# Kernel optimization log

Hardware: AMD Instinct MI355X
Metric: run time of the kernel (lower is better)

## Reference

```python
import jax, jax.numpy as jnp
import numpy as np

N = 100_000      # nodes
E = 1_600_000    # edges (avg degree 16)
D = 128          # emb_dim
L = 2            # num_layer
BN_EPS = 1e-5


def setup_inputs() -> dict:
    key = jax.random.key(0)
    ks = jax.random.split(key, 16)
    s = 0.05
    inp = {
        # int inputs
        "x": jax.random.randint(ks[0], (N, 9), 0, 2),
        "z": jax.random.randint(ks[1], (N,), 0, 1000),
        "edge_index": jax.random.randint(ks[2], (2, E), 0, N),
        "edge_attr": jax.random.randint(ks[3], (E, 3), 0, 2),
        # learned params
        "atom_emb": jax.random.normal(ks[4], (9, 119, D), jnp.float32) * s,  # padded stacked AtomEncoder tables
        "z_emb": jax.random.normal(ks[5], (1000, D), jnp.float32) * s,
        "bond_emb": jax.random.normal(ks[6], (L, 3, 6, D), jnp.float32) * s,  # padded BondEncoder tables per layer
        "eps": jnp.zeros((L,), jnp.float32),
        "W1": jax.random.normal(ks[7], (L, D, 2 * D), jnp.float32) * s,
        "b1": jnp.zeros((L, 2 * D), jnp.float32),
        "g1": jnp.ones((L, 2 * D), jnp.float32),
        "be1": jnp.zeros((L, 2 * D), jnp.float32),
        "W2": jax.random.normal(ks[8], (L, 2 * D, D), jnp.float32) * s,
        "b2": jnp.zeros((L, D), jnp.float32),
        "bng": jnp.ones((L, D), jnp.float32),
        "bnb": jnp.zeros((L, D), jnp.float32),
    }
    return inp


def _batchnorm(h, g, b):
    # training-mode BatchNorm1d: batch stats, biased variance
    m = h.mean(axis=0)
    v = h.var(axis=0)
    return (h - m) * jax.lax.rsqrt(v + BN_EPS) * g + b


def _multi_embed(tables, idx):
    # tables: [F, V, D], idx: [N, F] -> sum_f tables[f][idx[:, f]]  -> [N, D]
    return jax.vmap(lambda t, i: t[i], in_axes=(0, 1))(tables, idx).sum(axis=0)


def reference(x, z, edge_index, edge_attr, atom_emb, z_emb, bond_emb, eps,
              W1, b1, g1, be1, W2, b2, bng, bnb):
    src, dst = edge_index[0], edge_index[1]
    # h0 = AtomEncoder(x) + z_embedding(z)
    h = _multi_embed(atom_emb, x) + z_emb[z]
    for l in range(L):
        # GINConv: bond encode -> gather -> relu message -> scatter-add -> MLP
        e_emb = _multi_embed(bond_emb[l], edge_attr)          # [E, D]
        msg = jax.nn.relu(h[src] + e_emb)                      # [E, D]
        agg = jax.ops.segment_sum(msg, dst, num_segments=N)    # [N, D]
        pre = (1.0 + eps[l]) * h + agg
        hid = jax.nn.relu(_batchnorm(pre @ W1[l] + b1[l], g1[l], be1[l]))
        hconv = hid @ W2[l] + b2[l]
        h = _batchnorm(hconv, bng[l], bnb[l])
        if l < L - 1:
            h = jax.nn.relu(h)   # dropout ratio 0 -> identity
    return h
```

## Files before the change

### kernel.cpp

```cpp
#include <hip/hip_runtime.h>

#define D 128
#define BN_EPS 1e-5f
#define NSUB 1024
#define CAP2 2048

typedef __attribute__((ext_vector_type(8))) short short8;
typedef __attribute__((ext_vector_type(4))) float floatx4;

__device__ __forceinline__ float bf2f(unsigned short u) {
    unsigned int x = ((unsigned int)u) << 16;
    return __builtin_bit_cast(float, x);
}
__device__ __forceinline__ unsigned short f2bf(float f) {
    unsigned int x = __builtin_bit_cast(unsigned int, f);
    x = x + 0x7FFFu + ((x >> 16) & 1u);
    return (unsigned short)(x >> 16);
}

__global__ void node_init_kernel(const int* __restrict__ x, const int* __restrict__ z,
                                 const float* __restrict__ atom_emb,
                                 const float* __restrict__ z_emb,
                                 unsigned short* __restrict__ hb, int N) {
    int gid = blockIdx.x * blockDim.x + threadIdx.x;
    int node = gid >> 5;
    if (node >= N) return;
    int d0 = (gid & 31) * 4;
    float4 acc = *(const float4*)(z_emb + (size_t)z[node] * D + d0);
#pragma unroll
    for (int f = 0; f < 9; ++f) {
        int v = x[node * 9 + f];
        const float4 t = *(const float4*)(atom_emb + (size_t)(f * 119 + v) * D + d0);
        acc.x += t.x; acc.y += t.y; acc.z += t.z; acc.w += t.w;
    }
    ushort4 o;
    o.x = f2bf(acc.x); o.y = f2bf(acc.y); o.z = f2bf(acc.z); o.w = f2bf(acc.w);
    *(ushort4*)(hb + (size_t)node * D + d0) = o;
}

__global__ __launch_bounds__(256)
void partition1_kernel(const int* __restrict__ ei, const int* __restrict__ ea,
                       int2* __restrict__ l1, int* __restrict__ tail1,
                       int E, int N, int capE, int ntiles, int nblocks) {
    __shared__ int lcnt[8], lbase[8];
    const int tid = threadIdx.x;
    for (int tile = blockIdx.x; tile < ntiles; tile += nblocks) {
        const int tb = tile * 4096;
        if (tid < 8) lcnt[tid] = 0;
        __syncthreads();
        int mydst[16], mypay[16];
#pragma unroll
        for (int j = 0; j < 16; ++j) {
            int e = tb + j * 256 + tid;
            if (e < E) {
                int dst = ei[E + e];
                int c = (ea[3 * e] * 6 + ea[3 * e + 1]) * 6 + ea[3 * e + 2];
                mydst[j] = dst;
                mypay[j] = ei[e] | (c << 17);
                atomicAdd(&lcnt[(int)((8LL * dst) / N)], 1);
            } else {
                mydst[j] = -1;
            }
        }
        __syncthreads();
        if (tid < 8) {
            lbase[tid] = atomicAdd(&tail1[tid], lcnt[tid]);
            lcnt[tid] = 0;
        }
        __syncthreads();
#pragma unroll
        for (int j = 0; j < 16; ++j) {
            if (mydst[j] >= 0) {
                int s = (int)((8LL * mydst[j]) / N);
                int pos = lbase[s] + atomicAdd(&lcnt[s], 1);
                if (pos < capE) l1[(size_t)s * capE + pos] = make_int2(mydst[j], mypay[j]);
            }
        }
        __syncthreads();
    }
}

__global__ __launch_bounds__(256)
void partition2_kernel(const int2* __restrict__ l1, const int* __restrict__ tail1,
                       unsigned int* __restrict__ subL, int* __restrict__ tail2,
                       int N, int capE, int G) {
    __shared__ int lcnt[128], lbase[128];
    const int s = blockIdx.x & 7;
    const int g = blockIdx.x >> 3;
    const int tid = threadIdx.x;
    const int len = min(tail1[s], capE);
    const int2* src = l1 + (size_t)s * capE;
    for (int tb = g * 4096; tb < len; tb += G * 4096) {
        if (tid < 128) lcnt[tid] = 0;
        __syncthreads();
        int2 e[16];
        int sub[16];
#pragma unroll
        for (int j = 0; j < 16; ++j) {
            int i = tb + j * 256 + tid;
            if (i < len) {
                e[j] = src[i];
                sub[j] = (int)((1024LL * e[j].x) / N) - (s << 7);
                atomicAdd(&lcnt[sub[j]], 1);
            } else {
                sub[j] = -1;
            }
        }
        __syncthreads();
        if (tid < 128) {
            lbase[tid] = atomicAdd(&tail2[(s << 7) + tid], lcnt[tid]);
            lcnt[tid] = 0;
        }
        __syncthreads();
#pragma unroll
        for (int j = 0; j < 16; ++j) {
            if (sub[j] >= 0) {
                int k = (s << 7) + sub[j];
                int lo = (int)(((long long)k * N + 1023) >> 10);
                int pos = lbase[sub[j]] + atomicAdd(&lcnt[sub[j]], 1);
                if (pos < CAP2)
                    subL[(size_t)k * CAP2 + pos] =
                        (unsigned int)e[j].y | ((unsigned int)(e[j].x - lo) << 25);
            }
        }
        __syncthreads();
    }
}

__global__ __launch_bounds__(1024)
void subscan_kernel(const int* __restrict__ tail2, int* __restrict__ subbase,
                    int* __restrict__ offsets, int N) {
    const int tid = threadIdx.x, lane = tid & 63, wid = tid >> 6;
    int v = min(tail2[tid], CAP2);
    int s = v;
#pragma unroll
    for (int off = 1; off < 64; off <<= 1) {
        int t = __shfl_up(s, off, 64);
        if (lane >= off) s += t;
    }
    __shared__ int ws[16];
    if (lane == 63) ws[wid] = s;
    __syncthreads();
    if (wid == 0) {
        int w = (lane < 16) ? ws[lane] : 0;
#pragma unroll
        for (int off = 1; off < 16; off <<= 1) {
            int t = __shfl_up(w, off, 64);
            if (lane >= off) w += t;
        }
        if (lane < 16) ws[lane] = w;
    }
    __syncthreads();
    int excl = (wid ? ws[wid - 1] : 0) + s - v;
    subbase[tid] = excl;
    if (tid == 1023) offsets[N] = excl + v;
}

__global__ __launch_bounds__(256)
void csr_sort_kernel(const unsigned int* __restrict__ subL, const int* __restrict__ tail2,
                     const int* __restrict__ subbase, int* __restrict__ offsets,
                     int* __restrict__ bucket, int N) {
    const int k = blockIdx.x;
    const int tid = threadIdx.x, lane = tid & 63, wid = tid >> 6;
    const int len = min(tail2[k], CAP2);
    const int base = subbase[k];
    const int lo = (int)(((long long)k * N + 1023) >> 10);
    const int hi = (int)(((long long)(k + 1) * N + 1023) >> 10);
    const int nn = hi - lo;
    __shared__ int cnt[128], loff[128], wsum[4];
    __shared__ unsigned int sorted[CAP2];
    const unsigned int* src = subL + (size_t)k * CAP2;

    if (tid < 128) cnt[tid] = 0;
    __syncthreads();
    for (int i = tid; i < len; i += 256) atomicAdd(&cnt[src[i] >> 25], 1);
    __syncthreads();
    int v = (tid < 128) ? cnt[tid] : 0;
    int s = v;
#pragma unroll
    for (int off = 1; off < 64; off <<= 1) {
        int t = __shfl_up(s, off, 64);
        if (lane >= off) s += t;
    }
    if (lane == 63) wsum[wid] = s;
    __syncthreads();
    if (tid < 128) loff[tid] = ((wid == 1) ? wsum[0] : 0) + s - v;
    __syncthreads();
    if (tid < nn) offsets[lo + tid] = base + loff[tid];
    if (tid < 128) cnt[tid] = 0;
    __syncthreads();
    for (int i = tid; i < len; i += 256) {
        unsigned int e = src[i];
        int ld = e >> 25;
        int pos = loff[ld] + atomicAdd(&cnt[ld], 1);
        sorted[pos] = e & 0x1FFFFFFu;
    }
    __syncthreads();
    for (int i = tid; i < len; i += 256) bucket[base + i] = (int)sorted[i];
}

__global__ void comb_kernel(const float* __restrict__ bond_emb, unsigned short* __restrict__ comb) {
    int idx = blockIdx.x * 256 + threadIdx.x;
    if (idx >= 216 * D) return;
    int c = idx >> 7, d = idx & 127;
    int a0 = c / 36, a1 = (c / 6) % 6, a2 = c % 6;
    const float* b = bond_emb + (size_t)blockIdx.y * 3 * 6 * D;
    float v = b[(0 * 6 + a0) * D + d] + b[(1 * 6 + a1) * D + d] + b[(2 * 6 + a2) * D + d];
    comb[(size_t)blockIdx.y * 216 * D + idx] = f2bf(v);
}

__global__ void pack_w_kernel(const float* __restrict__ W, unsigned short* __restrict__ Wp,
                              int total, int logN) {
    int idx = blockIdx.x * 256 + threadIdx.x;
    if (idx >= total) return;
    int NCOLS = 1 << logN;
    int k = idx >> logN, n = idx & (NCOLS - 1);
    int k0 = k >> 5, kq = k & 31, q = kq >> 3, j = kq & 7;
    int t = n >> 4, ln = n & 15;
    size_t dest = (((size_t)k0 * (NCOLS >> 4) + t) << 9) + ((q << 4) + ln) * 8 + j;
    const float* Wl = W + (size_t)blockIdx.y * total;
    unsigned short* Wpl = Wp + (size_t)blockIdx.y * total;
    Wpl[dest] = f2bf(Wl[idx]);
}

__global__ __launch_bounds__(256)
void gather_reduce_kernel(const int* __restrict__ offsets, const int* __restrict__ bucket,
                          const unsigned short* __restrict__ comb,
                          const unsigned short* __restrict__ hb,
                          const float* __restrict__ eps_l,
                          unsigned short* __restrict__ pre, int N) {
    int gid = blockIdx.x * blockDim.x + threadIdx.x;
    int node = gid >> 4;
    if (node >= N) return;
    int d0 = (gid & 15) * 8;

    union U8 { int4 i; unsigned short u[8]; };
    float s = 1.0f + eps_l[0];
    float a[8];
    {
        U8 hv; hv.i = *(const int4*)(hb + (size_t)node * D + d0);
#pragma unroll
        for (int j = 0; j < 8; ++j) a[j] = bf2f(hv.u[j]) * s;
    }
    const int beg = offsets[node], end = offsets[node + 1];
    for (int p = beg; p < end; p += 4) {
        int rem = end - p;
        int pk0 = bucket[p];
        int pk1 = bucket[rem > 1 ? p + 1 : p];
        int pk2 = bucket[rem > 2 ? p + 2 : p];
        int pk3 = bucket[rem > 3 ? p + 3 : p];
        U8 h0, h1, h2, h3, c0, c1, c2, c3;
        h0.i = *(const int4*)(hb + (size_t)(pk0 & 0x1FFFF) * D + d0);
        c0.i = *(const int4*)(comb + (size_t)((pk0 >> 17) & 0xFF) * D + d0);
        h1.i = *(const int4*)(hb + (size_t)(pk1 & 0x1FFFF) * D + d0);
        c1.i = *(const int4*)(comb + (size_t)((pk1 >> 17) & 0xFF) * D + d0);
        h2.i = *(const int4*)(hb + (size_t)(pk2 & 0x1FFFF) * D + d0);
        c2.i = *(const int4*)(comb + (size_t)((pk2 >> 17) & 0xFF) * D + d0);
        h3.i = *(const int4*)(hb + (size_t)(pk3 & 0x1FFFF) * D + d0);
        c3.i = *(const int4*)(comb + (size_t)((pk3 >> 17) & 0xFF) * D + d0);
#pragma unroll
        for (int j = 0; j < 8; ++j) a[j] += fmaxf(bf2f(h0.u[j]) + bf2f(c0.u[j]), 0.0f);
        if (rem > 1) {
#pragma unroll
            for (int j = 0; j < 8; ++j) a[j] += fmaxf(bf2f(h1.u[j]) + bf2f(c1.u[j]), 0.0f);
        }
        if (rem > 2) {
#pragma unroll
            for (int j = 0; j < 8; ++j) a[j] += fmaxf(bf2f(h2.u[j]) + bf2f(c2.u[j]), 0.0f);
        }
        if (rem > 3) {
#pragma unroll
            for (int j = 0; j < 8; ++j) a[j] += fmaxf(bf2f(h3.u[j]) + bf2f(c3.u[j]), 0.0f);
        }
    }
    U8 o;
#pragma unroll
    for (int j = 0; j < 8; ++j) o.u[j] = f2bf(a[j]);
    *(int4*)(pre + (size_t)node * D + d0) = o.i;
}

template <int K, int NCOLS, int TRANSFORM, int OUTBF>
__global__ __launch_bounds__(256)
void mfma_gemm_kernel(const unsigned short* __restrict__ A,
                      const unsigned short* __restrict__ Wp,
                      const float* __restrict__ bias,
                      const float* __restrict__ tscale, const float* __restrict__ tshift,
                      unsigned short* __restrict__ Cbf, float* __restrict__ Cf,
                      float* __restrict__ partial, int M) {
    constexpr int NT = NCOLS / 16;
    constexpr int NCHUNK = K / 32;
    constexpr int CPP = NCHUNK / 2;
    __shared__ unsigned short Ws[16384];
    __shared__ float red[NCOLS * 2];

    const int tid = threadIdx.x;
    const int wave = tid >> 6, lane = tid & 63;
    const int quad = lane >> 4, ln = lane & 15;
    const int m_base = blockIdx.x * 64 + wave * 16;
    int arow = m_base + ln;
    if (arow >= M) arow = M - 1;
    const int kq = quad * 8;

    int4 araw[NCHUNK];
#pragma unroll
    for (int c = 0; c < NCHUNK; ++c)
        araw[c] = *(const int4*)(A + (size_t)arow * K + c * 32 + kq);

    for (int i = tid; i < NCOLS * 2; i += 256) red[i] = 0.f;

    floatx4 acc[NT];
#pragma unroll
    for (int t = 0; t < NT; ++t) acc[t] = (floatx4){0.f, 0.f, 0.f, 0.f};

#pragma unroll
    for (int ph = 0; ph < 2; ++ph) {
        if (ph) __syncthreads();
#pragma unroll
        for (int i = 0; i < 16384; i += 2048)
            *(int4*)&Ws[i + tid * 8] = *(const int4*)&Wp[ph * 16384 + i + tid * 8];
        __syncthreads();
#pragma unroll
        for (int cc = 0; cc < CPP; ++cc) {
            const int c = ph * CPP + cc;
            short8 afrag;
            if constexpr (TRANSFORM) {
                union { int4 i; unsigned short u[8]; } raw;
                raw.i = araw[c];
                const int kb = c * 32 + kq;
                float4 sc0 = *(const float4*)(tscale + kb);
                float4 sc1 = *(const float4*)(tscale + kb + 4);
                float4 sh0 = *(const float4*)(tshift + kb);
                float4 sh1 = *(const float4*)(tshift + kb + 4);
                union { short8 v; unsigned short u[8]; } au;
                au.u[0] = f2bf(fmaxf(bf2f(raw.u[0]) * sc0.x + sh0.x, 0.f));
                au.u[1] = f2bf(fmaxf(bf2f(raw.u[1]) * sc0.y + sh0.y, 0.f));
                au.u[2] = f2bf(fmaxf(bf2f(raw.u[2]) * sc0.z + sh0.z, 0.f));
                au.u[3] = f2bf(fmaxf(bf2f(raw.u[3]) * sc0.w + sh0.w, 0.f));
                au.u[4] = f2bf(fmaxf(bf2f(raw.u[4]) * sc1.x + sh1.x, 0.f));
                au.u[5] = f2bf(fmaxf(bf2f(raw.u[5]) * sc1.y + sh1.y, 0.f));
                au.u[6] = f2bf(fmaxf(bf2f(raw.u[6]) * sc1.z + sh1.z, 0.f));
                au.u[7] = f2bf(fmaxf(bf2f(raw.u[7]) * sc1.w + sh1.w, 0.f));
                afrag = au.v;
            } else {
                afrag = __builtin_bit_cast(short8, araw[c]);
            }
#pragma unroll
            for (int t = 0; t < NT; ++t) {
                short8 bfrag = *(const short8*)&Ws[(((cc * NT) + t) << 9) + lane * 8];
                acc[t] = __builtin_amdgcn_mfma_f32_16x16x32_bf16(afrag, bfrag, acc[t], 0, 0, 0);
            }
        }
    }

#pragma unroll
    for (int t = 0; t < NT; ++t) {
        int col = t * 16 + ln;
        float bv = bias[col];
        float sv = 0.f, qv = 0.f;
#pragma unroll
        for (int r = 0; r < 4; ++r) {
            int row = m_base + quad * 4 + r;
            if (row < M) {
                float v = acc[t][r] + bv;
                sv += v; qv += v * v;
                if constexpr (OUTBF) Cbf[(size_t)row * NCOLS + col] = f2bf(v);
                else                 Cf[(size_t)row * NCOLS + col] = v;
            }
        }
        sv += __shfl_xor(sv, 16, 64); sv += __shfl_xor(sv, 32, 64);
        qv += __shfl_xor(qv, 16, 64); qv += __shfl_xor(qv, 32, 64);
        if (quad == 0) {
            atomicAdd(&red[col], sv);
            atomicAdd(&red[NCOLS + col], qv);
        }
    }
    __syncthreads();
    float* pout = partial + (size_t)blockIdx.x * (NCOLS * 2);
    for (int i = tid; i < NCOLS * 2; i += 256) pout[i] = red[i];
}

template <int NCOLS>
__global__ __launch_bounds__(256)
void reduce_stats_kernel(const float* __restrict__ partial, int nb,
                         const float* __restrict__ g, const float* __restrict__ b,
                         float* __restrict__ scale, float* __restrict__ shift, float invN) {
    const int col = blockIdx.x;
    const int tid = threadIdx.x;
    float s = 0.f, q = 0.f;
    for (int bb = tid; bb < nb; bb += 256) {
        const float* p = partial + (size_t)bb * (NCOLS * 2);
        s += p[col];
        q += p[NCOLS + col];
    }
#pragma unroll
    for (int off = 32; off > 0; off >>= 1) {
        s += __shfl_xor(s, off, 64);
        q += __shfl_xor(q, off, 64);
    }
    __shared__ float ws[4], wq[4];
    if ((tid & 63) == 0) { ws[tid >> 6] = s; wq[tid >> 6] = q; }
    __syncthreads();
    if (tid == 0) {
        s = ws[0] + ws[1] + ws[2] + ws[3];
        q = wq[0] + wq[1] + wq[2] + wq[3];
        float mean = s * invN;
        float var = q * invN - mean * mean;
        float inv = 1.0f / sqrtf(var + BN_EPS);
        float sc = g[col] * inv;
        scale[col] = sc;
        shift[col] = b[col] - mean * sc;
    }
}

__global__ void bn_apply_kernel(const float* __restrict__ X, float* __restrict__ Yf,
                                unsigned short* __restrict__ Yb,
                                const float* __restrict__ scale, const float* __restrict__ shift,
                                int N, int mode) {
    int gid = blockIdx.x * blockDim.x + threadIdx.x;
    int node = gid >> 5;
    if (node >= N) return;
    int d0 = (gid & 31) * 4;
    float4 v = *(const float4*)(X + (size_t)node * D + d0);
    float4 sc = *(const float4*)(scale + d0);
    float4 sh = *(const float4*)(shift + d0);
    float4 o;
    o.x = v.x * sc.x + sh.x;
    o.y = v.y * sc.y + sh.y;
    o.z = v.z * sc.z + sh.z;
    o.w = v.w * sc.w + sh.w;
    if (mode == 0) {
        ushort4 ob;
        ob.x = f2bf(fmaxf(o.x, 0.f));
        ob.y = f2bf(fmaxf(o.y, 0.f));
        ob.z = f2bf(fmaxf(o.z, 0.f));
        ob.w = f2bf(fmaxf(o.w, 0.f));
        *(ushort4*)(Yb + (size_t)node * D + d0) = ob;
    } else {
        *(float4*)(Yf + (size_t)node * D + d0) = o;
    }
}

extern "C" void kernel_launch(void* const* d_in, const int* in_sizes, int n_in,
                              void* d_out, int out_size, void* d_ws, size_t ws_size,
                              hipStream_t stream) {
    const int*   x        = (const int*)d_in[0];
    const int*   z        = (const int*)d_in[1];
    const int*   ei       = (const int*)d_in[2];
    const int*   ea       = (const int*)d_in[3];
    const float* atom_emb = (const float*)d_in[4];
    const float* z_emb    = (const float*)d_in[5];
    const float* bond_emb = (const float*)d_in[6];
    const float* eps      = (const float*)d_in[7];
    const float* W1       = (const float*)d_in[8];
    const float* b1       = (const float*)d_in[9];
    const float* g1       = (const float*)d_in[10];
    const float* be1      = (const float*)d_in[11];
    const float* W2       = (const float*)d_in[12];
    const float* b2       = (const float*)d_in[13];
    const float* bng      = (const float*)d_in[14];
    const float* bnb      = (const float*)d_in[15];

    const int N = in_sizes[1];
    const int E = in_sizes[3] / 3;

    float* h = (float*)d_out;

    const int ngb = (N + 63) / 64;
    const int capE = E / 8 + E / 64;

    char* ws = (char*)d_ws;
    size_t off = 0;
    auto alloc = [&](size_t bytes) { void* p = ws + off; off += (bytes + 255) & ~(size_t)255; return p; };
    unsigned short* pre_bf = (unsigned short*)alloc((size_t)N * D * 2);
    unsigned short* extra  = (unsigned short*)alloc((size_t)N * D * 2);
    (void)extra;
    float* out2 = (float*)pre_bf;
    unsigned short* out1_bf = (unsigned short*)alloc((size_t)N * 2 * D * 2);
    unsigned short* hb      = (unsigned short*)alloc((size_t)N * D * 2);
    int* offsets = (int*)alloc((size_t)(N + 1) * 4);
    int* bucket  = (int*)alloc((size_t)E * 4);
    int2* l1     = (int2*)alloc((size_t)8 * capE * 8);
    unsigned int* subL = (unsigned int*)alloc((size_t)NSUB * CAP2 * 4);
    int* subbase = (int*)alloc(NSUB * 4);
    float* stats = (float*)alloc(1024 * 4);
    float* partial1 = (float*)alloc((size_t)ngb * 512 * 4);
    float* partial2 = (float*)alloc((size_t)ngb * 256 * 4);
    unsigned short* w1p  = (unsigned short*)alloc((size_t)2 * D * 2 * D * 2);
    unsigned short* w2p  = (unsigned short*)alloc((size_t)2 * 2 * D * D * 2);
    unsigned short* comb = (unsigned short*)alloc((size_t)2 * 216 * D * 2);
    int* tail1 = (int*)out1_bf;
    int* tail2 = tail1 + 8;

    float* scale1 = stats;
    float* shift1 = stats + 256;
    float* scale2 = stats + 512;
    float* shift2 = stats + 640;

    const float invN = 1.0f / (float)N;
    const int ntiles = (E + 4095) / 4096;

    hipMemsetAsync(tail1, 0, (8 + NSUB) * sizeof(int), stream);
    partition1_kernel<<<256, 256, 0, stream>>>(ei, ea, l1, tail1, E, N, capE, ntiles, 256);
    partition2_kernel<<<256, 256, 0, stream>>>(l1, tail1, subL, tail2, N, capE, 32);
    subscan_kernel<<<1, 1024, 0, stream>>>(tail2, subbase, offsets, N);
    csr_sort_kernel<<<NSUB, 256, 0, stream>>>(subL, tail2, subbase, offsets, bucket, N);

    node_init_kernel<<<(N * 32 + 255) / 256, 256, 0, stream>>>(x, z, atom_emb, z_emb, hb, N);
    comb_kernel<<<dim3((216 * D + 255) / 256, 2), 256, 0, stream>>>(bond_emb, comb);
    pack_w_kernel<<<dim3((D * 2 * D + 255) / 256, 2), 256, 0, stream>>>(W1, w1p, D * 2 * D, 8);
    pack_w_kernel<<<dim3((2 * D * D + 255) / 256, 2), 256, 0, stream>>>(W2, w2p, 2 * D * D, 7);

    for (int l = 0; l < 2; ++l) {
        gather_reduce_kernel<<<(N * 16 + 255) / 256, 256, 0, stream>>>(
            offsets, bucket, comb + (size_t)l * 216 * D, hb, eps + l, pre_bf, N);

        mfma_gemm_kernel<128, 256, 0, 1><<<ngb, 256, 0, stream>>>(
            pre_bf, w1p + (size_t)l * D * 2 * D, b1 + (size_t)l * 2 * D,
            nullptr, nullptr, out1_bf, nullptr, partial1, N);
        reduce_stats_kernel<256><<<256, 256, 0, stream>>>(
            partial1, ngb, g1 + (size_t)l * 2 * D, be1 + (size_t)l * 2 * D,
            scale1, shift1, invN);

        mfma_gemm_kernel<256, 128, 1, 0><<<ngb, 256, 0, stream>>>(
            out1_bf, w2p + (size_t)l * 2 * D * D, b2 + (size_t)l * D,
            scale1, shift1, nullptr, out2, partial2, N);
        reduce_stats_kernel<128><<<128, 256, 0, stream>>>(
            partial2, ngb, bng + (size_t)l * D, bnb + (size_t)l * D,
            scale2, shift2, invN);

        bn_apply_kernel<<<(N * 32 + 255) / 256, 256, 0, stream>>>(out2, h, hb, scale2, shift2,
                                                                  N, l == 0 ? 0 : 1);
    }
}
```

Before: 574.4 us.

## Merge setup kernels, use magic division, per-wave counters, bf16 layer-0 GEMM2 output

Folds node init, bond-combination and both weight-packing kernels into one launch to cut launch overhead. Replaces 64-bit integer division in the partition kernels with a magic-multiply shift. Splits the shared bucket counters per wave to reduce LDS atomic contention. Layer 0's second GEMM now writes bf16 instead of fp32, halving that intermediate's traffic at some precision cost before BN.

```diff
diff --git a/kernel.cpp b/kernel.cpp
--- a/kernel.cpp
+++ b/kernel.cpp
@@ -17,36 +17,70 @@
     x = x + 0x7FFFu + ((x >> 16) & 1u);
     return (unsigned short)(x >> 16);
 }
-
-__global__ void node_init_kernel(const int* __restrict__ x, const int* __restrict__ z,
-                                 const float* __restrict__ atom_emb,
-                                 const float* __restrict__ z_emb,
-                                 unsigned short* __restrict__ hb, int N) {
-    int gid = blockIdx.x * blockDim.x + threadIdx.x;
-    int node = gid >> 5;
-    if (node >= N) return;
-    int d0 = (gid & 31) * 4;
-    float4 acc = *(const float4*)(z_emb + (size_t)z[node] * D + d0);
-#pragma unroll
-    for (int f = 0; f < 9; ++f) {
-        int v = x[node * 9 + f];
-        const float4 t = *(const float4*)(atom_emb + (size_t)(f * 119 + v) * D + d0);
-        acc.x += t.x; acc.y += t.y; acc.z += t.z; acc.w += t.w;
-    }
-    ushort4 o;
-    o.x = f2bf(acc.x); o.y = f2bf(acc.y); o.z = f2bf(acc.z); o.w = f2bf(acc.w);
-    *(ushort4*)(hb + (size_t)node * D + d0) = o;
+__device__ __forceinline__ int magdiv(unsigned int x, unsigned long long magic) {
+    return (int)(((unsigned long long)x * magic) >> 44);
+}
+
+__global__ __launch_bounds__(256)
+void setup_kernel(const int* __restrict__ x, const int* __restrict__ z,
+                  const float* __restrict__ atom_emb, const float* __restrict__ z_emb,
+                  unsigned short* __restrict__ hb, int N, int nbNode,
+                  const float* __restrict__ bond_emb, unsigned short* __restrict__ comb,
+                  const float* __restrict__ W1, unsigned short* __restrict__ w1p,
+                  const float* __restrict__ W2, unsigned short* __restrict__ w2p) {
+    const int b = blockIdx.x;
+    const int tid = threadIdx.x;
+    if (b < nbNode) {
+        int gid = b * 256 + tid;
+        int node = gid >> 5;
+        if (node >= N) return;
+        int d0 = (gid & 31) * 4;
+        float4 acc = *(const float4*)(z_emb + (size_t)z[node] * D + d0);
+#pragma unroll
+        for (int f = 0; f < 9; ++f) {
+            int v = x[node * 9 + f];
+            const float4 t = *(const float4*)(atom_emb + (size_t)(f * 119 + v) * D + d0);
+            acc.x += t.x; acc.y += t.y; acc.z += t.z; acc.w += t.w;
+        }
+        ushort4 o;
+        o.x = f2bf(acc.x); o.y = f2bf(acc.y); o.z = f2bf(acc.z); o.w = f2bf(acc.w);
+        *(ushort4*)(hb + (size_t)node * D + d0) = o;
+    } else if (b < nbNode + 216) {
+        int t = (b - nbNode) * 256 + tid;
+        int layer = t / (216 * D);
+        int idx = t - layer * (216 * D);
+        int c = idx >> 7, d = idx & 127;
+        int a0 = c / 36, a1 = (c / 6) % 6, a2 = c % 6;
+        const float* bb = bond_emb + (size_t)layer * 3 * 6 * D;
+        float v = bb[(0 * 6 + a0) * D + d] + bb[(1 * 6 + a1) * D + d] + bb[(2 * 6 + a2) * D + d];
+        comb[(size_t)layer * 216 * D + idx] = f2bf(v);
+    } else {
+        int isW2 = (b >= nbNode + 216 + 256);
+        int t = (b - nbNode - 216 - (isW2 ? 256 : 0)) * 256 + tid;
+        int layer = t >> 15;
+        int idx = t & 32767;
+        int logN = isW2 ? 7 : 8;
+        int NCOLS = 1 << logN;
+        int k = idx >> logN, n = idx & (NCOLS - 1);
+        int k0 = k >> 5, kq = k & 31, q = kq >> 3, j = kq & 7;
+        int tt = n >> 4, ln = n & 15;
+        size_t dest = (((size_t)k0 * (NCOLS >> 4) + tt) << 9) + ((q << 4) + ln) * 8 + j;
+        const float* W = (isW2 ? W2 : W1) + (size_t)layer * 32768;
+        unsigned short* Wp = (isW2 ? w2p : w1p) + (size_t)layer * 32768;
+        Wp[dest] = f2bf(W[idx]);
+    }
 }
 
 __global__ __launch_bounds__(256)
 void partition1_kernel(const int* __restrict__ ei, const int* __restrict__ ea,
                        int2* __restrict__ l1, int* __restrict__ tail1,
-                       int E, int N, int capE, int ntiles, int nblocks) {
-    __shared__ int lcnt[8], lbase[8];
+                       int E, unsigned long long magic, int capE, int ntiles, int nblocks) {
+    __shared__ int lcnt[4][8], lbase[4][8];
     const int tid = threadIdx.x;
+    const int wid = tid >> 6;
     for (int tile = blockIdx.x; tile < ntiles; tile += nblocks) {
         const int tb = tile * 4096;
-        if (tid < 8) lcnt[tid] = 0;
+        if (tid < 32) ((int*)lcnt)[tid] = 0;
         __syncthreads();
         int mydst[16], mypay[16];
 #pragma unroll
@@ -57,22 +91,23 @@
                 int c = (ea[3 * e] * 6 + ea[3 * e + 1]) * 6 + ea[3 * e + 2];
                 mydst[j] = dst;
                 mypay[j] = ei[e] | (c << 17);
-                atomicAdd(&lcnt[(int)((8LL * dst) / N)], 1);
+                atomicAdd(&lcnt[wid][magdiv((unsigned)dst * 8u, magic)], 1);
             } else {
                 mydst[j] = -1;
             }
         }
         __syncthreads();
-        if (tid < 8) {
-            lbase[tid] = atomicAdd(&tail1[tid], lcnt[tid]);
-            lcnt[tid] = 0;
+        if (tid < 32) {
+            int w = tid >> 3, s = tid & 7;
+            lbase[w][s] = atomicAdd(&tail1[s], lcnt[w][s]);
+            lcnt[w][s] = 0;
         }
         __syncthreads();
 #pragma unroll
         for (int j = 0; j < 16; ++j) {
             if (mydst[j] >= 0) {
-                int s = (int)((8LL * mydst[j]) / N);
-                int pos = lbase[s] + atomicAdd(&lcnt[s], 1);
+                int s = magdiv((unsigned)mydst[j] * 8u, magic);
+                int pos = lbase[wid][s] + atomicAdd(&lcnt[wid][s], 1);
                 if (pos < capE) l1[(size_t)s * capE + pos] = make_int2(mydst[j], mypay[j]);
             }
         }
@@ -83,7 +118,7 @@
 __global__ __launch_bounds__(256)
 void partition2_kernel(const int2* __restrict__ l1, const int* __restrict__ tail1,
                        unsigned int* __restrict__ subL, int* __restrict__ tail2,
-                       int N, int capE, int G) {
+                       int N, unsigned long long magic, int capE, int G) {
     __shared__ int lcnt[128], lbase[128];
     const int s = blockIdx.x & 7;
     const int g = blockIdx.x >> 3;
@@ -100,7 +135,7 @@
             int i = tb + j * 256 + tid;
             if (i < len) {
                 e[j] = src[i];
-                sub[j] = (int)((1024LL * e[j].x) / N) - (s << 7);
+                sub[j] = magdiv((unsigned)e[j].x * 1024u, magic) - (s << 7);
                 atomicAdd(&lcnt[sub[j]], 1);
             } else {
                 sub[j] = -1;
@@ -197,30 +232,6 @@
     }
     __syncthreads();
     for (int i = tid; i < len; i += 256) bucket[base + i] = (int)sorted[i];
-}
-
-__global__ void comb_kernel(const float* __restrict__ bond_emb, unsigned short* __restrict__ comb) {
-    int idx = blockIdx.x * 256 + threadIdx.x;
-    if (idx >= 216 * D) return;
-    int c = idx >> 7, d = idx & 127;
-    int a0 = c / 36, a1 = (c / 6) % 6, a2 = c % 6;
-    const float* b = bond_emb + (size_t)blockIdx.y * 3 * 6 * D;
-    float v = b[(0 * 6 + a0) * D + d] + b[(1 * 6 + a1) * D + d] + b[(2 * 6 + a2) * D + d];
-    comb[(size_t)blockIdx.y * 216 * D + idx] = f2bf(v);
-}
-
-__global__ void pack_w_kernel(const float* __restrict__ W, unsigned short* __restrict__ Wp,
-                              int total, int logN) {
-    int idx = blockIdx.x * 256 + threadIdx.x;
-    if (idx >= total) return;
-    int NCOLS = 1 << logN;
-    int k = idx >> logN, n = idx & (NCOLS - 1);
-    int k0 = k >> 5, kq = k & 31, q = kq >> 3, j = kq & 7;
-    int t = n >> 4, ln = n & 15;
-    size_t dest = (((size_t)k0 * (NCOLS >> 4) + t) << 9) + ((q << 4) + ln) * 8 + j;
-    const float* Wl = W + (size_t)blockIdx.y * total;
-    unsigned short* Wpl = Wp + (size_t)blockIdx.y * total;
-    Wpl[dest] = f2bf(Wl[idx]);
 }
 
 __global__ __launch_bounds__(256)
@@ -412,15 +423,21 @@
     }
 }
 
-__global__ void bn_apply_kernel(const float* __restrict__ X, float* __restrict__ Yf,
-                                unsigned short* __restrict__ Yb,
+__global__ void bn_apply_kernel(const float* __restrict__ Xf, const unsigned short* __restrict__ Xb,
+                                float* __restrict__ Yf, unsigned short* __restrict__ Yb,
                                 const float* __restrict__ scale, const float* __restrict__ shift,
                                 int N, int mode) {
     int gid = blockIdx.x * blockDim.x + threadIdx.x;
     int node = gid >> 5;
     if (node >= N) return;
     int d0 = (gid & 31) * 4;
-    float4 v = *(const float4*)(X + (size_t)node * D + d0);
+    float4 v;
+    if (mode == 0) {
+        ushort4 b = *(const ushort4*)(Xb + (size_t)node * D + d0);
+        v.x = bf2f(b.x); v.y = bf2f(b.y); v.z = bf2f(b.z); v.w = bf2f(b.w);
+    } else {
+        v = *(const float4*)(Xf + (size_t)node * D + d0);
+    }
     float4 sc = *(const float4*)(scale + d0);
     float4 sh = *(const float4*)(shift + d0);
     float4 o;
@@ -467,6 +484,7 @@
 
     const int ngb = (N + 63) / 64;
     const int capE = E / 8 + E / 64;
+    const unsigned long long magic = ((1ULL << 44) / (unsigned int)N) + 1;
 
     char* ws = (char*)d_ws;
     size_t off = 0;
@@ -475,6 +493,7 @@
     unsigned short* extra  = (unsigned short*)alloc((size_t)N * D * 2);
     (void)extra;
     float* out2 = (float*)pre_bf;
+    unsigned short* out2_bf = pre_bf;
     unsigned short* out1_bf = (unsigned short*)alloc((size_t)N * 2 * D * 2);
     unsigned short* hb      = (unsigned short*)alloc((size_t)N * D * 2);
     int* offsets = (int*)alloc((size_t)(N + 1) * 4);
@@ -498,17 +517,16 @@
 
     const float invN = 1.0f / (float)N;
     const int ntiles = (E + 4095) / 4096;
+    const int nbNode = (N * 32 + 255) / 256;
 
     hipMemsetAsync(tail1, 0, (8 + NSUB) * sizeof(int), stream);
-    partition1_kernel<<<256, 256, 0, stream>>>(ei, ea, l1, tail1, E, N, capE, ntiles, 256);
-    partition2_kernel<<<256, 256, 0, stream>>>(l1, tail1, subL, tail2, N, capE, 32);
+    partition1_kernel<<<256, 256, 0, stream>>>(ei, ea, l1, tail1, E, magic, capE, ntiles, 256);
+    partition2_kernel<<<256, 256, 0, stream>>>(l1, tail1, subL, tail2, N, magic, capE, 32);
     subscan_kernel<<<1, 1024, 0, stream>>>(tail2, subbase, offsets, N);
     csr_sort_kernel<<<NSUB, 256, 0, stream>>>(subL, tail2, subbase, offsets, bucket, N);
 
-    node_init_kernel<<<(N * 32 + 255) / 256, 256, 0, stream>>>(x, z, atom_emb, z_emb, hb, N);
-    comb_kernel<<<dim3((216 * D + 255) / 256, 2), 256, 0, stream>>>(bond_emb, comb);
-    pack_w_kernel<<<dim3((D * 2 * D + 255) / 256, 2), 256, 0, stream>>>(W1, w1p, D * 2 * D, 8);
-    pack_w_kernel<<<dim3((2 * D * D + 255) / 256, 2), 256, 0, stream>>>(W2, w2p, 2 * D * D, 7);
+    setup_kernel<<<nbNode + 216 + 256 + 256, 256, 0, stream>>>(
+        x, z, atom_emb, z_emb, hb, N, nbNode, bond_emb, comb, W1, w1p, W2, w2p);
 
     for (int l = 0; l < 2; ++l) {
         gather_reduce_kernel<<<(N * 16 + 255) / 256, 256, 0, stream>>>(
@@ -521,14 +539,20 @@
             partial1, ngb, g1 + (size_t)l * 2 * D, be1 + (size_t)l * 2 * D,
             scale1, shift1, invN);
 
-        mfma_gemm_kernel<256, 128, 1, 0><<<ngb, 256, 0, stream>>>(
-            out1_bf, w2p + (size_t)l * 2 * D * D, b2 + (size_t)l * D,
-            scale1, shift1, nullptr, out2, partial2, N);
+        if (l == 0) {
+            mfma_gemm_kernel<256, 128, 1, 1><<<ngb, 256, 0, stream>>>(
+                out1_bf, w2p + (size_t)l * 2 * D * D, b2 + (size_t)l * D,
+                scale1, shift1, out2_bf, nullptr, partial2, N);
+        } else {
+            mfma_gemm_kernel<256, 128, 1, 0><<<ngb, 256, 0, stream>>>(
+                out1_bf, w2p + (size_t)l * 2 * D * D, b2 + (size_t)l * D,
+                scale1, shift1, nullptr, out2, partial2, N);
+        }
         reduce_stats_kernel<128><<<128, 256, 0, stream>>>(
             partial2, ngb, bng + (size_t)l * D, bnb + (size_t)l * D,
             scale2, shift2, invN);
 
-        bn_apply_kernel<<<(N * 32 + 255) / 256, 256, 0, stream>>>(out2, h, hb, scale2, shift2,
-                                                                  N, l == 0 ? 0 : 1);
-    }
-}
+        bn_apply_kernel<<<(N * 32 + 255) / 256, 256, 0, stream>>>(
+            out2, out2_bf, h, hb, scale2, shift2, N, l == 0 ? 0 : 1);
+    }
+}
```

After: 574.7 us. About the same (+0.0%).
